# Kernel tuning notes

Hardware: AMD Instinct MI355X
Metric: run time of the kernel (lower is better)

The kernel has to match this reference:

```python
import jax, jax.numpy as jnp
import numpy as np

E, TOPK, H, I = 8, 2, 2048, 5632
T = 4096


def setup_inputs() -> dict:
    key = jax.random.key(0)
    k1, k2, k3, k4 = jax.random.split(key, 4)
    hidden_states = jax.random.normal(k1, (T, H), dtype=jnp.float32)
    gate_w = jax.random.normal(k2, (E, H), dtype=jnp.float32) * (1.0 / np.sqrt(H))
    # fused gate+up projection: [E, 2*I, H]
    w13 = jax.random.normal(k3, (E, 2 * I, H), dtype=jnp.float32) * (1.0 / np.sqrt(H))
    # down projection: [E, H, I]
    w2 = jax.random.normal(k4, (E, H, I), dtype=jnp.float32) * (1.0 / np.sqrt(I))
    return {"hidden_states": hidden_states, "gate_w": gate_w, "w13": w13, "w2": w2, "top_k": TOPK}


def reference(hidden_states, gate_w, w13, w2, top_k):
    num_experts = gate_w.shape[0]
    inter = w2.shape[2]
    # router: fp32 gate logits -> softmax -> top-k -> renormalize (FusedMoE renormalize=True)
    logits = hidden_states.astype(jnp.float32) @ gate_w.T          # [T, E]
    probs = jax.nn.softmax(logits, axis=-1)
    vals, idx = jax.lax.top_k(probs, top_k)                        # [T, k]
    vals = vals / jnp.sum(vals, axis=-1, keepdims=True)
    # dense routing weight matrix [T, E] (zero outside top-k)
    dense_w = jnp.sum(jax.nn.one_hot(idx, num_experts, dtype=vals.dtype) * vals[..., None], axis=1)

    def body(acc, inputs):
        w13_e, w2_e, we = inputs                                   # [2I,H], [H,I], [T]
        gu = hidden_states @ w13_e.T                               # [T, 2I]
        g, u = gu[:, :inter], gu[:, inter:]
        h = jax.nn.silu(g) * u                                     # SwiGLU
        y = h @ w2_e.T                                             # [T, H]
        return acc + we[:, None] * y, None

    acc0 = jnp.zeros_like(hidden_states)
    out, _ = jax.lax.scan(body, acc0, (w13, w2, dense_w.T))
    return out
```

## Files before the change

### kernel.cpp

```cpp
#include <hip/hip_runtime.h>

#define T_TOK 4096
#define H_DIM 2048
#define I_DIM 5632
#define NE 8

typedef _Float16 f16;
typedef _Float16 f16x8 __attribute__((ext_vector_type(8)));
typedef _Float16 f16x4 __attribute__((ext_vector_type(4)));
typedef float f32x4 __attribute__((ext_vector_type(4)));

#define OFF_META   0
#define OFF_BTOK   256
#define OFF_BW     (256 + 32768)
#define OFF_RE     (256 + 2 * 32768)
#define OFF_RW     (256 + 3 * 32768)
#define OFF_HSB    (256 + 4 * 32768)
#define OFF_HB     (OFF_HSB + (size_t)T_TOK * H_DIM * 2)

typedef const __attribute__((address_space(1))) unsigned int guint;
typedef __attribute__((address_space(3))) unsigned int luint;

#define WAITLG0()  asm volatile("s_waitcnt lgkmcnt(0)" ::: "memory")

__device__ __forceinline__ int swzk(int r, int bir) {
    return (bir & 15) | ((((bir >> 4) ^ r) & 7) << 4);
}

__device__ __forceinline__ f16x4 cvt4(float4 v) {
    f16x4 t; t[0] = (f16)v.x; t[1] = (f16)v.y; t[2] = (f16)v.z; t[3] = (f16)v.w; return t;
}

__global__ void cvt_hs_kernel(const float* __restrict__ hs, f16* __restrict__ hsb) {
    size_t i = ((size_t)blockIdx.x * 256 + threadIdx.x) * 8;
    float4 a = *(const float4*)(hs + i);
    float4 b = *(const float4*)(hs + i + 4);
    f16x8 v;
    v[0] = (f16)a.x; v[1] = (f16)a.y; v[2] = (f16)a.z; v[3] = (f16)a.w;
    v[4] = (f16)b.x; v[5] = (f16)b.y; v[6] = (f16)b.z; v[7] = (f16)b.w;
    *(f16x8*)(hsb + i) = v;
}

__global__ void gate_kernel(const float* __restrict__ hs, const float* __restrict__ gw,
                            int* __restrict__ re, float* __restrict__ rw,
                            int* __restrict__ counts) {
    int lane = threadIdx.x & 63;
    int t = blockIdx.x * 4 + (threadIdx.x >> 6);
    float acc[NE];
#pragma unroll
    for (int e = 0; e < NE; ++e) acc[e] = 0.f;
    const float* x = hs + (size_t)t * H_DIM;
    for (int i = lane; i < H_DIM; i += 64) {
        float xv = x[i];
#pragma unroll
        for (int e = 0; e < NE; ++e) acc[e] += xv * gw[e * H_DIM + i];
    }
#pragma unroll
    for (int e = 0; e < NE; ++e)
        for (int off = 32; off > 0; off >>= 1) acc[e] += __shfl_xor(acc[e], off);
    if (lane == 0) {
        int i1 = 0; float l1 = acc[0];
#pragma unroll
        for (int e = 1; e < NE; ++e) if (acc[e] > l1) { l1 = acc[e]; i1 = e; }
        int i2 = -1; float l2 = -1e30f;
#pragma unroll
        for (int e = 0; e < NE; ++e) if (e != i1 && acc[e] > l2) { l2 = acc[e]; i2 = e; }
        float aa = __expf(l2 - l1);
        float s = 1.f / (1.f + aa);
        re[t * 2] = i1; re[t * 2 + 1] = i2;
        rw[t * 2] = s;  rw[t * 2 + 1] = aa * s;
        atomicAdd(&counts[i1], 1);
        atomicAdd(&counts[i2], 1);
    }
}

__global__ void scan_kernel(int* __restrict__ meta) {
    if (threadIdx.x == 0) {
        int s = 0;
        for (int e = 0; e < NE; ++e) { meta[8 + e] = s; meta[16 + e] = s; s += meta[e]; }
    }
}

__global__ void place_kernel(const int* __restrict__ re, const float* __restrict__ rw,
                             int* __restrict__ cursor, int* __restrict__ btok,
                             float* __restrict__ bwv) {
    int t = blockIdx.x * 256 + threadIdx.x;
    if (t >= T_TOK) return;
#pragma unroll
    for (int s = 0; s < 2; ++s) {
        int e = re[t * 2 + s];
        int p = atomicAdd(&cursor[e], 1);
        btok[p] = t;
        bwv[p] = rw[t * 2 + s];
    }
}

__device__ __forceinline__ void decode_panel(int id, int npx, int e_arg,
                                             int& e, int& bx, int& by) {
    int sg  = id >> 7;
    int rem = id & 127;
    by = rem >> 3;
    int P = sg * 8 + (rem & 7);
    if (e_arg >= 0) { e = e_arg; bx = P; }
    else            { e = P / npx; bx = P % npx; }
}

__global__ __launch_bounds__(512, 4) void gemm1_kernel(
    const float* __restrict__ w13, const f16* __restrict__ hsb, f16* __restrict__ hb,
    const int* __restrict__ counts, const int* __restrict__ offs,
    const int* __restrict__ btok, int e_arg, int global_h)
{
    int e, bx, by;
    decode_panel(blockIdx.x, 88, e_arg, e, bx, by);
    const int n_e = counts[e];
    if (by * 256 >= n_e) return;
    const int boff = offs[e];
    const float* We = w13 + (size_t)e * (2 * I_DIM) * H_DIM;

    const int tid = threadIdx.x;
    const int lane = tid & 63;
    const int wid = tid >> 6;
    const int wm = wid >> 1;
    const int wn = wid & 1;

    __shared__ f16 As[2][256 * 64];
    __shared__ f16 Bg[64 * 64];
    __shared__ f16 Bu[64 * 64];
    char* AsB = (char*)As; char* BgB = (char*)Bg; char* BuB = (char*)Bu;

    const f16* gA[4];
    int adst[4];
#pragma unroll
    for (int i = 0; i < 4; ++i) {
        int c = i * 512 + tid;
        int r = c >> 3;
        int idx = by * 256 + r;
        idx = idx < n_e ? idx : n_e - 1;
        int tok = btok[boff + idx];
        int sg = (c & 7) ^ (r & 7);
        gA[i] = hsb + (size_t)tok * H_DIM + sg * 8;
        adst[i] = c * 16;
    }
    const float* gBg[2]; const float* gBu[2];
    int bwadr[2];
#pragma unroll
    for (int j = 0; j < 2; ++j) {
        int c = j * 512 + tid;
        int r = c >> 4;
        int k4 = c & 15;
        gBg[j] = We + (size_t)(bx * 64 + r) * H_DIM + k4 * 4;
        gBu[j] = We + (size_t)(I_DIM + bx * 64 + r) * H_DIM + k4 * 4;
        bwadr[j] = r * 128 + swzk(r, k4 * 8);
    }

    f32x4 accg[4][2], accu[4][2];
#pragma unroll
    for (int m = 0; m < 4; ++m)
#pragma unroll
        for (int n = 0; n < 2; ++n) { accg[m][n] = (f32x4)0.f; accu[m][n] = (f32x4)0.f; }

    const int NT = H_DIM / 64;

    float4 gR[2], uR[2];
#pragma unroll
    for (int i = 0; i < 4; ++i)
        __builtin_amdgcn_global_load_lds((guint*)(gA[i]), (luint*)(AsB + adst[i]), 16, 0, 0);
#pragma unroll
    for (int j = 0; j < 2; ++j) { gR[j] = *(const float4*)gBg[j]; uR[j] = *(const float4*)gBu[j]; }

    int cur = 0;
#pragma unroll 1
    for (int kt = 0; kt < NT; ++kt) {
        WAITLG0();
        __builtin_amdgcn_s_barrier();
#pragma unroll
        for (int j = 0; j < 2; ++j) {
            *(f16x4*)(BgB + bwadr[j]) = cvt4(gR[j]);
            *(f16x4*)(BuB + bwadr[j]) = cvt4(uR[j]);
        }
        if (kt + 1 < NT) {
            int k0 = (kt + 1) * 64;
#pragma unroll
            for (int i = 0; i < 4; ++i)
                __builtin_amdgcn_global_load_lds((guint*)(gA[i] + k0),
                    (luint*)(AsB + (cur ^ 1) * 32768 + adst[i]), 16, 0, 0);
        }
        WAITLG0();
        __builtin_amdgcn_s_barrier();
        if (kt + 1 < NT) {
            int k0 = (kt + 1) * 64;
#pragma unroll
            for (int j = 0; j < 2; ++j) {
                gR[j] = *(const float4*)(gBg[j] + k0);
                uR[j] = *(const float4*)(gBu[j] + k0);
            }
        }
        const char* Ab = AsB + cur * 32768;
#pragma unroll
        for (int kh = 0; kh < 2; ++kh) {
            f16x8 a[4], bg[2], bu[2];
            const int kb = kh * 64 + (lane >> 4) * 16;
#pragma unroll
            for (int m = 0; m < 4; ++m) {
                int r = wm * 64 + m * 16 + (lane & 15);
                a[m] = *(const f16x8*)(Ab + r * 128 + swzk(r, kb));
            }
#pragma unroll
            for (int n = 0; n < 2; ++n) {
                int r = wn * 32 + n * 16 + (lane & 15);
                bg[n] = *(const f16x8*)(BgB + r * 128 + swzk(r, kb));
                bu[n] = *(const f16x8*)(BuB + r * 128 + swzk(r, kb));
            }
#pragma unroll
            for (int m = 0; m < 4; ++m)
#pragma unroll
                for (int n = 0; n < 2; ++n) {
                    accg[m][n] = __builtin_amdgcn_mfma_f32_16x16x32_f16(a[m], bg[n], accg[m][n], 0, 0, 0);
                    accu[m][n] = __builtin_amdgcn_mfma_f32_16x16x32_f16(a[m], bu[n], accu[m][n], 0, 0, 0);
                }
        }
        cur ^= 1;
    }

    const int hbase = (global_h ? boff : 0) + by * 256;
#pragma unroll
    for (int m = 0; m < 4; ++m) {
        int rl0 = wm * 64 + m * 16 + ((lane >> 4) << 2);
#pragma unroll
        for (int r = 0; r < 4; ++r) {
            int rl = rl0 + r;
            if (by * 256 + rl < n_e) {
#pragma unroll
                for (int n = 0; n < 2; ++n) {
                    float g = accg[m][n][r];
                    float u = accu[m][n][r];
                    float h = g / (1.f + __expf(-g)) * u;
                    hb[(size_t)(hbase + rl) * I_DIM + bx * 64 + wn * 32 + n * 16 + (lane & 15)] = (f16)h;
                }
            }
        }
    }
}

__global__ __launch_bounds__(512, 4) void gemm2_kernel(
    const float* __restrict__ w2, const f16* __restrict__ hb, float* __restrict__ out,
    const int* __restrict__ counts, const int* __restrict__ offs,
    const int* __restrict__ btok, const float* __restrict__ bwv, int e_arg, int global_h)
{
    int e, bx, by;
    decode_panel(blockIdx.x, 16, e_arg, e, bx, by);
    const int n_e = counts[e];
    if (by * 256 >= n_e) return;
    const int boff = offs[e];
    const float* We = w2 + (size_t)e * H_DIM * I_DIM;

    const int tid = threadIdx.x;
    const int lane = tid & 63;
    const int wid = tid >> 6;
    const int wm = wid >> 1;
    const int wn = wid & 1;

    __shared__ f16 As[2][256 * 64];
    __shared__ f16 Bs[128 * 64];
    char* AsB = (char*)As; char* BsB = (char*)Bs;

    const int hbase = (global_h ? boff : 0) + by * 256;
    const f16* gA[4];
    int adst[4];
#pragma unroll
    for (int i = 0; i < 4; ++i) {
        int c = i * 512 + tid;
        int r = c >> 3;
        int sg = (c & 7) ^ (r & 7);
        gA[i] = hb + (size_t)(hbase + r) * I_DIM + sg * 8;
        adst[i] = c * 16;
    }
    const float* gB[4];
    int bwadr[4];
#pragma unroll
    for (int j = 0; j < 4; ++j) {
        int c = j * 512 + tid;
        int r = c >> 4;
        int k4 = c & 15;
        gB[j] = We + (size_t)(bx * 128 + r) * I_DIM + k4 * 4;
        bwadr[j] = r * 128 + swzk(r, k4 * 8);
    }

    f32x4 acc[4][4];
#pragma unroll
    for (int m = 0; m < 4; ++m)
#pragma unroll
        for (int n = 0; n < 4; ++n) acc[m][n] = (f32x4)0.f;

    const int NT = I_DIM / 64;

    float4 bR[4];
#pragma unroll
    for (int i = 0; i < 4; ++i)
        __builtin_amdgcn_global_load_lds((guint*)(gA[i]), (luint*)(AsB + adst[i]), 16, 0, 0);
#pragma unroll
    for (int j = 0; j < 4; ++j) bR[j] = *(const float4*)gB[j];

    int cur = 0;
#pragma unroll 1
    for (int kt = 0; kt < NT; ++kt) {
        WAITLG0();
        __builtin_amdgcn_s_barrier();
#pragma unroll
        for (int j = 0; j < 4; ++j) *(f16x4*)(BsB + bwadr[j]) = cvt4(bR[j]);
        if (kt + 1 < NT) {
            int k0 = (kt + 1) * 64;
#pragma unroll
            for (int i = 0; i < 4; ++i)
                __builtin_amdgcn_global_load_lds((guint*)(gA[i] + k0),
                    (luint*)(AsB + (cur ^ 1) * 32768 + adst[i]), 16, 0, 0);
        }
        WAITLG0();
        __builtin_amdgcn_s_barrier();
        if (kt + 1 < NT) {
            int k0 = (kt + 1) * 64;
#pragma unroll
            for (int j = 0; j < 4; ++j) bR[j] = *(const float4*)(gB[j] + k0);
        }
        const char* Ab = AsB + cur * 32768;
#pragma unroll
        for (int kh = 0; kh < 2; ++kh) {
            f16x8 a[4], b[4];
            const int kb = kh * 64 + (lane >> 4) * 16;
#pragma unroll
            for (int m = 0; m < 4; ++m) {
                int r = wm * 64 + m * 16 + (lane & 15);
                a[m] = *(const f16x8*)(Ab + r * 128 + swzk(r, kb));
            }
#pragma unroll
            for (int n = 0; n < 4; ++n) {
                int r = wn * 64 + n * 16 + (lane & 15);
                b[n] = *(const f16x8*)(BsB + r * 128 + swzk(r, kb));
            }
#pragma unroll
            for (int m = 0; m < 4; ++m)
#pragma unroll
                for (int n = 0; n < 4; ++n)
                    acc[m][n] = __builtin_amdgcn_mfma_f32_16x16x32_f16(a[m], b[n], acc[m][n], 0, 0, 0);
        }
        cur ^= 1;
    }

#pragma unroll
    for (int m = 0; m < 4; ++m) {
        int rl0 = wm * 64 + m * 16 + ((lane >> 4) << 2);
#pragma unroll
        for (int r = 0; r < 4; ++r) {
            int rl = rl0 + r;
            if (by * 256 + rl < n_e) {
                int p = boff + by * 256 + rl;
                int tok = btok[p];
                float w = bwv[p];
#pragma unroll
                for (int n = 0; n < 4; ++n)
                    atomicAdd(&out[(size_t)tok * H_DIM + bx * 128 + wn * 64 + n * 16 + (lane & 15)],
                              w * acc[m][n][r]);
            }
        }
    }
}

extern "C" void kernel_launch(void* const* d_in, const int* in_sizes, int n_in,
                              void* d_out, int out_size, void* d_ws, size_t ws_size,
                              hipStream_t stream) {
    const float* hs  = (const float*)d_in[0];
    const float* gw  = (const float*)d_in[1];
    const float* w13 = (const float*)d_in[2];
    const float* w2  = (const float*)d_in[3];
    float* out = (float*)d_out;

    char* ws = (char*)d_ws;
    int*   meta = (int*)(ws + OFF_META);
    int*   btok = (int*)(ws + OFF_BTOK);
    float* bwv  = (float*)(ws + OFF_BW);
    int*   re   = (int*)(ws + OFF_RE);
    float* rw   = (float*)(ws + OFF_RW);
    f16*   hsb  = (f16*)(ws + OFF_HSB);
    f16*   hb   = (f16*)(ws + OFF_HB);

    hipMemsetAsync(d_out, 0, (size_t)T_TOK * H_DIM * 4, stream);
    hipMemsetAsync(meta, 0, 256, stream);

    cvt_hs_kernel<<<(T_TOK * H_DIM) / (256 * 8), 256, 0, stream>>>(hs, hsb);
    gate_kernel<<<T_TOK / 4, 256, 0, stream>>>(hs, gw, re, rw, meta);
    scan_kernel<<<1, 64, 0, stream>>>(meta);
    place_kernel<<<T_TOK / 256, 256, 0, stream>>>(re, rw, meta + 16, btok, bwv);

    size_t need_allpairs = OFF_HB + (size_t)(2 * T_TOK + 256) * I_DIM * 2;
    if (ws_size >= need_allpairs) {
        gemm1_kernel<<<704 * 16, 512, 0, stream>>>(w13, hsb, hb, meta, meta + 8, btok, -1, 1);
        gemm2_kernel<<<128 * 16, 512, 0, stream>>>(w2, hb, out, meta, meta + 8, btok, bwv, -1, 1);
    } else {
        for (int e = 0; e < NE; ++e) {
            gemm1_kernel<<<88 * 16, 512, 0, stream>>>(w13, hsb, hb, meta, meta + 8, btok, e, 0);
            gemm2_kernel<<<16 * 16, 512, 0, stream>>>(w2, hb, out, meta, meta + 8, btok, bwv, e, 0);
        }
    }
}
```

Before: 1.354 ms.

## Double-buffer weight tiles and deepen prefetch with single barrier per K-step

Both MoE GEMM kernels now double-buffer the converted weight tiles in LDS and keep two register sets of fp32 weight prefetches, two K-tiles ahead. Each K-step needs one barrier instead of two, and waits use vmcnt-based partial waits so global loads stay in flight during the MFMA work. MFMA sections run at raised wave priority, and launch bounds drop from 4 to 2 waves per SIMD to leave room for the extra registers. This costs more LDS and registers, and it lowers potential occupancy.

```diff
diff --git a/kernel.cpp b/kernel.cpp
--- a/kernel.cpp
+++ b/kernel.cpp
@@ -21,7 +21,10 @@
 typedef const __attribute__((address_space(1))) unsigned int guint;
 typedef __attribute__((address_space(3))) unsigned int luint;
 
-#define WAITLG0()  asm volatile("s_waitcnt lgkmcnt(0)" ::: "memory")
+#define WAITVM4()  do { asm volatile("s_waitcnt vmcnt(4)" ::: "memory"); __builtin_amdgcn_sched_barrier(0); } while (0)
+#define WAITVM0()  do { asm volatile("s_waitcnt vmcnt(0)" ::: "memory"); __builtin_amdgcn_sched_barrier(0); } while (0)
+#define WAITLG0()  do { asm volatile("s_waitcnt lgkmcnt(0)" ::: "memory"); __builtin_amdgcn_sched_barrier(0); } while (0)
+#define BARRIER()  do { __builtin_amdgcn_s_barrier(); __builtin_amdgcn_sched_barrier(0); } while (0)
 
 __device__ __forceinline__ int swzk(int r, int bir) {
     return (bir & 15) | ((((bir >> 4) ^ r) & 7) << 4);
@@ -105,7 +108,7 @@
     else            { e = P / npx; bx = P % npx; }
 }
 
-__global__ __launch_bounds__(512, 4) void gemm1_kernel(
+__global__ __launch_bounds__(512, 2) void gemm1_kernel(
     const float* __restrict__ w13, const f16* __restrict__ hsb, f16* __restrict__ hb,
     const int* __restrict__ counts, const int* __restrict__ offs,
     const int* __restrict__ btok, int e_arg, int global_h)
@@ -124,8 +127,8 @@
     const int wn = wid & 1;
 
     __shared__ f16 As[2][256 * 64];
-    __shared__ f16 Bg[64 * 64];
-    __shared__ f16 Bu[64 * 64];
+    __shared__ f16 Bg[2][64 * 64];
+    __shared__ f16 Bu[2][64 * 64];
     char* AsB = (char*)As; char* BgB = (char*)Bg; char* BuB = (char*)Bu;
 
     const f16* gA[4];
@@ -161,66 +164,89 @@
 
     const int NT = H_DIM / 64;
 
-    float4 gR[2], uR[2];
+    float4 gRa[2], uRa[2], gRb[2], uRb[2];
+
 #pragma unroll
     for (int i = 0; i < 4; ++i)
         __builtin_amdgcn_global_load_lds((guint*)(gA[i]), (luint*)(AsB + adst[i]), 16, 0, 0);
 #pragma unroll
-    for (int j = 0; j < 2; ++j) { gR[j] = *(const float4*)gBg[j]; uR[j] = *(const float4*)gBu[j]; }
+    for (int j = 0; j < 2; ++j) { gRb[j] = *(const float4*)gBg[j]; uRb[j] = *(const float4*)gBu[j]; }
+#pragma unroll
+    for (int j = 0; j < 2; ++j) { gRa[j] = *(const float4*)(gBg[j] + 64); uRa[j] = *(const float4*)(gBu[j] + 64); }
+    WAITVM4();
+#pragma unroll
+    for (int j = 0; j < 2; ++j) {
+        *(f16x4*)(BgB + bwadr[j]) = cvt4(gRb[j]);
+        *(f16x4*)(BuB + bwadr[j]) = cvt4(uRb[j]);
+    }
+    WAITLG0();
+    BARRIER();
 
     int cur = 0;
+
+#define G1_TILE(t, bIg, bIu, bSg, bSu)                                              \
+    {                                                                               \
+        const int kA = (((t) + 1 < NT) ? (t) + 1 : NT - 1) * 64;                    \
+        const int kB = (((t) + 2 < NT) ? (t) + 2 : NT - 1) * 64;                    \
+        _Pragma("unroll")                                                           \
+        for (int i = 0; i < 4; ++i)                                                 \
+            __builtin_amdgcn_global_load_lds((guint*)(gA[i] + kA),                  \
+                (luint*)(AsB + (cur ^ 1) * 32768 + adst[i]), 16, 0, 0);             \
+        _Pragma("unroll")                                                           \
+        for (int j = 0; j < 2; ++j) {                                               \
+            bIg[j] = *(const float4*)(gBg[j] + kB);                                 \
+            bIu[j] = *(const float4*)(gBu[j] + kB);                                 \
+        }                                                                           \
+        const char* Ab = AsB + cur * 32768;                                         \
+        const char* Gb = BgB + cur * 8192;                                          \
+        const char* Ub = BuB + cur * 8192;                                          \
+        __builtin_amdgcn_s_setprio(1);                                              \
+        _Pragma("unroll")                                                           \
+        for (int kh = 0; kh < 2; ++kh) {                                            \
+            f16x8 a[4], bg[2], bu[2];                                               \
+            const int kb = kh * 64 + (lane >> 4) * 16;                              \
+            _Pragma("unroll")                                                       \
+            for (int m = 0; m < 4; ++m) {                                           \
+                int r = wm * 64 + m * 16 + (lane & 15);                             \
+                a[m] = *(const f16x8*)(Ab + r * 128 + swzk(r, kb));                 \
+            }                                                                       \
+            _Pragma("unroll")                                                       \
+            for (int n = 0; n < 2; ++n) {                                           \
+                int r = wn * 32 + n * 16 + (lane & 15);                             \
+                bg[n] = *(const f16x8*)(Gb + r * 128 + swzk(r, kb));                \
+                bu[n] = *(const f16x8*)(Ub + r * 128 + swzk(r, kb));                \
+            }                                                                       \
+            _Pragma("unroll")                                                       \
+            for (int m = 0; m < 4; ++m)                                             \
+                _Pragma("unroll")                                                   \
+                for (int n = 0; n < 2; ++n) {                                       \
+                    accg[m][n] = __builtin_amdgcn_mfma_f32_16x16x32_f16(a[m], bg[n], accg[m][n], 0, 0, 0); \
+                    accu[m][n] = __builtin_amdgcn_mfma_f32_16x16x32_f16(a[m], bu[n], accu[m][n], 0, 0, 0); \
+                }                                                                   \
+        }                                                                           \
+        __builtin_amdgcn_s_setprio(0);                                              \
+        WAITVM4();              \
+        {                                                                           \
+            char* Gn = BgB + (cur ^ 1) * 8192;                                      \
+            char* Un = BuB + (cur ^ 1) * 8192;                                      \
+            _Pragma("unroll")                                                       \
+            for (int j = 0; j < 2; ++j) {                                           \
+                *(f16x4*)(Gn + bwadr[j]) = cvt4(bSg[j]);                            \
+                *(f16x4*)(Un + bwadr[j]) = cvt4(bSu[j]);                            \
+            }                                                                       \
+        }                                                                           \
+        WAITLG0();                                                                  \
+        BARRIER();                                                                  \
+        cur ^= 1;                                                                   \
+    }
+
 #pragma unroll 1
-    for (int kt = 0; kt < NT; ++kt) {
-        WAITLG0();
-        __builtin_amdgcn_s_barrier();
-#pragma unroll
-        for (int j = 0; j < 2; ++j) {
-            *(f16x4*)(BgB + bwadr[j]) = cvt4(gR[j]);
-            *(f16x4*)(BuB + bwadr[j]) = cvt4(uR[j]);
-        }
-        if (kt + 1 < NT) {
-            int k0 = (kt + 1) * 64;
-#pragma unroll
-            for (int i = 0; i < 4; ++i)
-                __builtin_amdgcn_global_load_lds((guint*)(gA[i] + k0),
-                    (luint*)(AsB + (cur ^ 1) * 32768 + adst[i]), 16, 0, 0);
-        }
-        WAITLG0();
-        __builtin_amdgcn_s_barrier();
-        if (kt + 1 < NT) {
-            int k0 = (kt + 1) * 64;
-#pragma unroll
-            for (int j = 0; j < 2; ++j) {
-                gR[j] = *(const float4*)(gBg[j] + k0);
-                uR[j] = *(const float4*)(gBu[j] + k0);
-            }
-        }
-        const char* Ab = AsB + cur * 32768;
-#pragma unroll
-        for (int kh = 0; kh < 2; ++kh) {
-            f16x8 a[4], bg[2], bu[2];
-            const int kb = kh * 64 + (lane >> 4) * 16;
-#pragma unroll
-            for (int m = 0; m < 4; ++m) {
-                int r = wm * 64 + m * 16 + (lane & 15);
-                a[m] = *(const f16x8*)(Ab + r * 128 + swzk(r, kb));
-            }
-#pragma unroll
-            for (int n = 0; n < 2; ++n) {
-                int r = wn * 32 + n * 16 + (lane & 15);
-                bg[n] = *(const f16x8*)(BgB + r * 128 + swzk(r, kb));
-                bu[n] = *(const f16x8*)(BuB + r * 128 + swzk(r, kb));
-            }
-#pragma unroll
-            for (int m = 0; m < 4; ++m)
-#pragma unroll
-                for (int n = 0; n < 2; ++n) {
-                    accg[m][n] = __builtin_amdgcn_mfma_f32_16x16x32_f16(a[m], bg[n], accg[m][n], 0, 0, 0);
-                    accu[m][n] = __builtin_amdgcn_mfma_f32_16x16x32_f16(a[m], bu[n], accu[m][n], 0, 0, 0);
-                }
-        }
-        cur ^= 1;
-    }
+    for (int kt = 0; kt < NT; kt += 2) {
+        G1_TILE(kt,     gRb, uRb, gRa, uRa);
+        G1_TILE(kt + 1, gRa, uRa, gRb, uRb);
+    }
+#undef G1_TILE
+    WAITVM0();
 
     const int hbase = (global_h ? boff : 0) + by * 256;
 #pragma unroll
@@ -242,7 +268,7 @@
     }
 }
 
-__global__ __launch_bounds__(512, 4) void gemm2_kernel(
+__global__ __launch_bounds__(512, 2) void gemm2_kernel(
     const float* __restrict__ w2, const f16* __restrict__ hb, float* __restrict__ out,
     const int* __restrict__ counts, const int* __restrict__ offs,
     const int* __restrict__ btok, const float* __restrict__ bwv, int e_arg, int global_h)
@@ -261,7 +287,7 @@
     const int wn = wid & 1;
 
     __shared__ f16 As[2][256 * 64];
-    __shared__ f16 Bs[128 * 64];
+    __shared__ f16 Bs[2][128 * 64];
     char* AsB = (char*)As; char* BsB = (char*)Bs;
 
     const int hbase = (global_h ? boff : 0) + by * 256;
@@ -294,57 +320,75 @@
 
     const int NT = I_DIM / 64;
 
-    float4 bR[4];
+    float4 bRa[4], bRb[4];
+
 #pragma unroll
     for (int i = 0; i < 4; ++i)
         __builtin_amdgcn_global_load_lds((guint*)(gA[i]), (luint*)(AsB + adst[i]), 16, 0, 0);
 #pragma unroll
-    for (int j = 0; j < 4; ++j) bR[j] = *(const float4*)gB[j];
+    for (int j = 0; j < 4; ++j) bRb[j] = *(const float4*)gB[j];
+#pragma unroll
+    for (int j = 0; j < 4; ++j) bRa[j] = *(const float4*)(gB[j] + 64);
+    WAITVM4();
+#pragma unroll
+    for (int j = 0; j < 4; ++j) *(f16x4*)(BsB + bwadr[j]) = cvt4(bRb[j]);
+    WAITLG0();
+    BARRIER();
 
     int cur = 0;
+
+#define G2_TILE(t, bI, bS)                                                          \
+    {                                                                               \
+        const int kA = (((t) + 1 < NT) ? (t) + 1 : NT - 1) * 64;                    \
+        const int kB = (((t) + 2 < NT) ? (t) + 2 : NT - 1) * 64;                    \
+        _Pragma("unroll")                                                           \
+        for (int i = 0; i < 4; ++i)                                                 \
+            __builtin_amdgcn_global_load_lds((guint*)(gA[i] + kA),                  \
+                (luint*)(AsB + (cur ^ 1) * 32768 + adst[i]), 16, 0, 0);             \
+        _Pragma("unroll")                                                           \
+        for (int j = 0; j < 4; ++j) bI[j] = *(const float4*)(gB[j] + kB);           \
+        const char* Ab = AsB + cur * 32768;                                         \
+        const char* Bb = BsB + cur * 16384;                                         \
+        __builtin_amdgcn_s_setprio(1);                                              \
+        _Pragma("unroll")                                                           \
+        for (int kh = 0; kh < 2; ++kh) {                                            \
+            f16x8 a[4], b[4];                                                       \
+            const int kb = kh * 64 + (lane >> 4) * 16;                              \
+            _Pragma("unroll")                                                       \
+            for (int m = 0; m < 4; ++m) {                                           \
+                int r = wm * 64 + m * 16 + (lane & 15);                             \
+                a[m] = *(const f16x8*)(Ab + r * 128 + swzk(r, kb));                 \
+            }                                                                       \
+            _Pragma("unroll")                                                       \
+            for (int n = 0; n < 4; ++n) {                                           \
+                int r = wn * 64 + n * 16 + (lane & 15);                             \
+                b[n] = *(const f16x8*)(Bb + r * 128 + swzk(r, kb));                 \
+            }                                                                       \
+            _Pragma("unroll")                                                       \
+            for (int m = 0; m < 4; ++m)                                             \
+                _Pragma("unroll")                                                   \
+                for (int n = 0; n < 4; ++n)                                         \
+                    acc[m][n] = __builtin_amdgcn_mfma_f32_16x16x32_f16(a[m], b[n], acc[m][n], 0, 0, 0); \
+        }                                                                           \
+        __builtin_amdgcn_s_setprio(0);                                              \
+        WAITVM4();                                                                  \
+        {                                                                           \
+            char* Bn = BsB + (cur ^ 1) * 16384;                                     \
+            _Pragma("unroll")                                                       \
+            for (int j = 0; j < 4; ++j) *(f16x4*)(Bn + bwadr[j]) = cvt4(bS[j]);     \
+        }                                                                           \
+        WAITLG0();                                                                  \
+        BARRIER();                                                                  \
+        cur ^= 1;                                                                   \
+    }
+
 #pragma unroll 1
-    for (int kt = 0; kt < NT; ++kt) {
-        WAITLG0();
-        __builtin_amdgcn_s_barrier();
-#pragma unroll
-        for (int j = 0; j < 4; ++j) *(f16x4*)(BsB + bwadr[j]) = cvt4(bR[j]);
-        if (kt + 1 < NT) {
-            int k0 = (kt + 1) * 64;
-#pragma unroll
-            for (int i = 0; i < 4; ++i)
-                __builtin_amdgcn_global_load_lds((guint*)(gA[i] + k0),
-                    (luint*)(AsB + (cur ^ 1) * 32768 + adst[i]), 16, 0, 0);
-        }
-        WAITLG0();
-        __builtin_amdgcn_s_barrier();
-        if (kt + 1 < NT) {
-            int k0 = (kt + 1) * 64;
-#pragma unroll
-            for (int j = 0; j < 4; ++j) bR[j] = *(const float4*)(gB[j] + k0);
-        }
-        const char* Ab = AsB + cur * 32768;
-#pragma unroll
-        for (int kh = 0; kh < 2; ++kh) {
-            f16x8 a[4], b[4];
-            const int kb = kh * 64 + (lane >> 4) * 16;
-#pragma unroll
-            for (int m = 0; m < 4; ++m) {
-                int r = wm * 64 + m * 16 + (lane & 15);
-                a[m] = *(const f16x8*)(Ab + r * 128 + swzk(r, kb));
-            }
-#pragma unroll
-            for (int n = 0; n < 4; ++n) {
-                int r = wn * 64 + n * 16 + (lane & 15);
-                b[n] = *(const f16x8*)(BsB + r * 128 + swzk(r, kb));
-            }
-#pragma unroll
-            for (int m = 0; m < 4; ++m)
-#pragma unroll
-                for (int n = 0; n < 4; ++n)
-                    acc[m][n] = __builtin_amdgcn_mfma_f32_16x16x32_f16(a[m], b[n], acc[m][n], 0, 0, 0);
-        }
-        cur ^= 1;
-    }
+    for (int kt = 0; kt < NT; kt += 2) {
+        G2_TILE(kt,     bRb, bRa);
+        G2_TILE(kt + 1, bRa, bRb);
+    }
+#undef G2_TILE
+    WAITVM0();
 
 #pragma unroll
     for (int m = 0; m < 4; ++m) {
```

New measurement: 1.437 ms. 1.06x slower.
